# Performance work log

Measured on AMD Instinct MI355X. Metric: run time of the kernel, lower is better.

Reference implementation:

```python
import jax, jax.numpy as jnp
import numpy as np

N = 100000   # nodes
E = 1600000  # edges
IN, HID, OUT = 128, 128, 64


def setup_inputs() -> dict:
    key = jax.random.key(0)
    ks = jax.random.split(key, 8)
    x = jax.random.normal(ks[0], (N, IN), dtype=jnp.float32)
    edge_index = jax.random.randint(ks[1], (2, E), 0, N, dtype=jnp.int64)
    W1 = jax.random.normal(ks[2], (IN, HID), dtype=jnp.float32) * 0.05
    b1 = jnp.zeros((HID,), dtype=jnp.float32)
    W2 = jax.random.normal(ks[3], (HID, OUT), dtype=jnp.float32) * 0.05
    b2 = jnp.zeros((OUT,), dtype=jnp.float32)
    Wd = jax.random.normal(ks[4], (OUT, IN), dtype=jnp.float32) * 0.05
    bd = jnp.zeros((IN,), dtype=jnp.float32)
    return {"x": x, "edge_index": edge_index, "W1": W1, "b1": b1,
            "W2": W2, "b2": b2, "Wd": Wd, "bd": bd}


def _gcn_conv(x, src, dst, W, b):
    # PyG GCNConv: add self-loops, symmetric normalization D^-1/2 (A+I) D^-1/2,
    # messages flow src -> dst, aggregated by sum at dst.
    h = x @ W                                   # [N, F]
    ones = jnp.ones((src.shape[0],), x.dtype)
    deg = jax.ops.segment_sum(ones, dst, num_segments=N) + 1.0  # +1 for self-loop
    dinv = jax.lax.rsqrt(deg)                   # deg^-1/2, [N]
    coef = dinv[src] * dinv[dst]                # per-edge norm
    agg = jax.ops.segment_sum(h[src] * coef[:, None], dst, num_segments=N)
    agg = agg + h * (dinv * dinv)[:, None]      # self-loop contribution
    return agg + b


def reference(x, edge_index, W1, b1, W2, b2, Wd, bd):
    src, dst = edge_index[0], edge_index[1]
    h = jax.nn.relu(_gcn_conv(x, src, dst, W1, b1))
    # dropout in eval mode -> identity
    z = _gcn_conv(h, src, dst, W2, b2)          # [N, OUT] embedding
    x_recon = z @ Wd + bd                        # [N, IN]
    return (x_recon, z)
```

## Files before the change

kernel.cpp:

```cpp
#include <hip/hip_runtime.h>
#include <hip/hip_bf16.h>
#include <hip/hip_fp16.h>


#define TPB 256
#define CAP 64
#define BINCAP 220000
#define FILLW 112

typedef float v2f __attribute__((ext_vector_type(2)));


__device__ __forceinline__ unsigned short f2bf(float f) {
    unsigned u = __float_as_uint(f);
    unsigned r = u + 0x7fffu + ((u >> 16) & 1u);
    return (unsigned short)(r >> 16);
}
__device__ __forceinline__ float bf_lo(unsigned u) { return __uint_as_float(u << 16); }
__device__ __forceinline__ float bf_hi(unsigned u) { return __uint_as_float(u & 0xffff0000u); }


template <int K, int C, int TN, bool BIAS, bool INBF, bool OUTBF>
__device__ __forceinline__ void gemm_body(const void* __restrict__ Ap,
                                          const float* __restrict__ W,
                                          const float* __restrict__ bias,
                                          void* __restrict__ outp, int N, int bid,
                                          float* __restrict__ Ws) {
    constexpr int BM  = 128;
    constexpr int TM  = 8;
    constexpr int BK  = 32;
    constexpr int NCT = C / TN;
    static_assert(NCT * (BM / TM) == TPB, "thread layout");

    int tid = threadIdx.x;
    int tc = tid % NCT;
    int tr = tid / NCT;
    int c0 = tc * TN;
    int r0 = bid * BM + tr * TM;

    float acc[TM][TN] = {};

    for (int k0 = 0; k0 < K; k0 += BK) {
        __syncthreads();
        for (int i = tid * 4; i < BK * C; i += TPB * 4)
            *(float4*)&Ws[i] = *(const float4*)&W[k0 * C + i];
        __syncthreads();

        for (int k = 0; k < BK; k += 4) {
            float4 a[TM];
            uint2  au[TM];
#pragma unroll
            for (int i = 0; i < TM; ++i) {
                int r = r0 + i;
                if (r >= N) r = N - 1;
                if (INBF)
                    au[i] = *(const uint2*)((const unsigned short*)Ap + (size_t)r * K + k0 + k);
                else
                    a[i] = *(const float4*)((const float*)Ap + (size_t)r * K + k0 + k);
            }
#pragma unroll
            for (int kk = 0; kk < 4; ++kk) {
                float w[TN];
#pragma unroll
                for (int j = 0; j < TN; j += 4)
                    *(float4*)&w[j] = *(const float4*)&Ws[(k + kk) * C + c0 + j];
#pragma unroll
                for (int i = 0; i < TM; ++i) {
                    float av;
                    if (INBF) {
                        unsigned uu = (kk < 2) ? au[i].x : au[i].y;
                        av = (kk & 1) ? bf_hi(uu) : bf_lo(uu);
                    } else {
                        av = ((const float*)&a[i])[kk];
                    }
#pragma unroll
                    for (int j = 0; j < TN; ++j) acc[i][j] += av * w[j];
                }
            }
        }
    }

#pragma unroll
    for (int i = 0; i < TM; ++i) {
        int r = r0 + i;
        if (r >= N) continue;
        if (BIAS) {
#pragma unroll
            for (int j = 0; j < TN; ++j) acc[i][j] += bias[c0 + j];
        }
        if (OUTBF) {
            unsigned short* ob = (unsigned short*)outp + (size_t)r * C + c0;
            unsigned pk[TN / 2];
#pragma unroll
            for (int j = 0; j < TN; j += 2)
                pk[j / 2] = (unsigned)f2bf(acc[i][j]) | ((unsigned)f2bf(acc[i][j + 1]) << 16);
            if (TN == 8)      *(uint4*)ob = *(uint4*)pk;
            else if (TN == 4) *(uint2*)ob = *(uint2*)pk;
        } else {
            float* of = (float*)outp + (size_t)r * C + c0;
#pragma unroll
            for (int j = 0; j < TN; j += 4)
                *(float4*)&of[j] = *(float4*)&acc[i][j];
        }
    }
}

template <int K, int C, int TN, bool BIAS, bool INBF, bool OUTBF>
__global__ __launch_bounds__(TPB) void gemm_k(const void* __restrict__ Ap,
                                              const float* __restrict__ W,
                                              const float* __restrict__ bias,
                                              void* __restrict__ outp, int N) {
    __shared__ float Ws[32 * C];
    gemm_body<K, C, TN, BIAS, INBF, OUTBF>(Ap, W, bias, outp, N, blockIdx.x, Ws);
}


__global__ __launch_bounds__(TPB) void fused1_k(const float* __restrict__ x,
                                                const float* __restrict__ W1,
                                                unsigned* __restrict__ h1b,
                                                const int* __restrict__ src,
                                                const int* __restrict__ dst,
                                                uint2* __restrict__ binBuf,
                                                int* __restrict__ binCnt,
                                                int N, int E, int gb, unsigned M) {
    __shared__ float Ws[32 * 128];
    __shared__ int hist[8], gbase[8], lpos[8];
    if ((int)blockIdx.x < gb) {
        gemm_body<128, 128, 8, false, false, true>(x, W1, nullptr, h1b, N, blockIdx.x, Ws);
    } else {
        int bid = (int)blockIdx.x - gb;
        int tid = (int)threadIdx.x;
        if (tid < 8) { hist[tid] = 0; lpos[tid] = 0; }
        __syncthreads();

        int e0 = (bid * TPB + tid) * 8;
        int ne = E - e0; ne = ne > 8 ? 8 : (ne < 0 ? 0 : ne);
        int ss[8], dd[8], bb8[8];
        if (ne == 8) {
            int4 sa = *(const int4*)&src[e0];
            int4 sb = *(const int4*)&src[e0 + 4];
            int4 da = *(const int4*)&dst[e0];
            int4 db = *(const int4*)&dst[e0 + 4];
            ss[0]=sa.x; ss[1]=sa.y; ss[2]=sa.z; ss[3]=sa.w;
            ss[4]=sb.x; ss[5]=sb.y; ss[6]=sb.z; ss[7]=sb.w;
            dd[0]=da.x; dd[1]=da.y; dd[2]=da.z; dd[3]=da.w;
            dd[4]=db.x; dd[5]=db.y; dd[6]=db.z; dd[7]=db.w;
        } else {
            for (int q = 0; q < ne; ++q) { ss[q] = src[e0 + q]; dd[q] = dst[e0 + q]; }
        }
        for (int q = 0; q < ne; ++q) {
            bb8[q] = (int)(((unsigned long long)(unsigned)dd[q] * M) >> 32);
            atomicAdd(&hist[bb8[q]], 1);
        }
        __syncthreads();
        if (tid < 8) gbase[tid] = atomicAdd(&binCnt[tid], hist[tid]);
        __syncthreads();
        for (int q = 0; q < ne; ++q) {
            int b = bb8[q];
            int p = gbase[b] + atomicAdd(&lpos[b], 1);
            if (p < BINCAP)
                binBuf[(size_t)b * BINCAP + p] = make_uint2((unsigned)ss[q], (unsigned)dd[q]);
        }
    }
}


__global__ __launch_bounds__(TPB) void fill_k(const uint2* __restrict__ binBuf,
                                              const int* __restrict__ binCnt,
                                              int* __restrict__ cnt,
                                              unsigned* __restrict__ bucket, int N) {
    int bin = (int)blockIdx.x & 7;
    int w   = (int)blockIdx.x >> 3;
    int cb  = binCnt[bin];
    if (cb > BINCAP) cb = BINCAP;
    const uint2* eb = binBuf + (size_t)bin * BINCAP;

    for (int base = w * (TPB * 8); base < cb; base += FILLW * (TPB * 8)) {
        int e0 = base + (int)threadIdx.x * 8;
        if (e0 + 8 <= cb) {
            unsigned s[8], d[8];
#pragma unroll
            for (int q = 0; q < 8; q += 2) {
                uint4 t = *(const uint4*)&eb[e0 + q];
                s[q] = t.x; d[q] = t.y; s[q + 1] = t.z; d[q + 1] = t.w;
            }
            int rr[8];
#pragma unroll
            for (int q = 0; q < 8; ++q) rr[q] = atomicAdd(&cnt[(int)d[q]], 1);
#pragma unroll
            for (int q = 0; q < 8; ++q)
                if (rr[q] < CAP) bucket[(size_t)rr[q] * N + d[q]] = s[q];
        } else {
            int lim = e0 + 8 < cb ? e0 + 8 : cb;
            for (int e = e0; e < lim; ++e) {
                uint2 t = eb[e];
                int r = atomicAdd(&cnt[(int)t.y], 1);
                if (r < CAP) bucket[(size_t)r * N + t.y] = t.x;
            }
        }
    }
}


__global__ __launch_bounds__(TPB) void dinv_k(const int* __restrict__ cnt,
                                              float* __restrict__ dinv, int N) {
    int i = blockIdx.x * TPB + (int)threadIdx.x;
    if (i < N) dinv[i] = rsqrtf((float)cnt[i] + 1.0f);
}


template <int F2, bool RELU, bool OUTBF>
__global__ __launch_bounds__(TPB) void agg_k(const unsigned* __restrict__ h,
                                             const float* __restrict__ dinv,
                                             const int* __restrict__ cnt,
                                             const unsigned* __restrict__ bucket,
                                             const float* __restrict__ bias,
                                             void* __restrict__ outp, int N) {
    constexpr int NPB = TPB / F2;
    int ln = threadIdx.x / F2;
    int f2 = threadIdx.x % F2;
    int n  = blockIdx.x * NPB + ln;
    if (n >= N) return;

    int cfull = cnt[n];
    float di = dinv[n];
    const unsigned* hp = h + f2;
    unsigned us = hp[(size_t)n * F2];
    v2f acc;
    acc.x = bf_lo(us) * (di * di);
    acc.y = bf_hi(us) * (di * di);

    int cn = cfull < CAP ? cfull : CAP;
    const unsigned* bp = bucket + n;

    int nfull = cn & ~7;
    int s[8], sn2[8];
    if (nfull > 0) {
#pragma unroll
        for (int q = 0; q < 8; ++q) s[q] = (int)bp[(size_t)q * N];
    }
    for (int j = 0; j < nfull; ) {
        int jn = j + 8;
        bool more = jn < nfull;
        if (more) {
#pragma unroll
            for (int q = 0; q < 8; ++q) sn2[q] = (int)bp[(size_t)(jn + q) * N];
        }
        unsigned v[8];
        float ds[8];
#pragma unroll
        for (int q = 0; q < 8; ++q) {
            v[q]  = hp[(size_t)s[q] * F2];
            ds[q] = dinv[s[q]];
        }
#pragma unroll
        for (int q = 0; q < 8; ++q) {
            float c = ds[q] * di;
            v2f hv; hv.x = bf_lo(v[q]); hv.y = bf_hi(v[q]);
            acc += hv * c;
        }
        if (more) {
#pragma unroll
            for (int q = 0; q < 8; ++q) s[q] = sn2[q];
        }
        j = jn;
    }
    for (int j = nfull; j < cn; ++j) {
        int sx = (int)bp[(size_t)j * N];
        unsigned v = hp[(size_t)sx * F2];
        float c = dinv[sx] * di;
        acc.x += c * bf_lo(v);
        acc.y += c * bf_hi(v);
    }

    float rx = acc.x + bias[2 * f2];
    float ry = acc.y + bias[2 * f2 + 1];
    if (RELU) { rx = fmaxf(rx, 0.f); ry = fmaxf(ry, 0.f); }
    if (OUTBF) {
        unsigned pk = (unsigned)f2bf(rx) | ((unsigned)f2bf(ry) << 16);
        ((unsigned*)outp)[(size_t)n * F2 + f2] = pk;
    } else {
        v2f r; r.x = rx; r.y = ry;
        __builtin_nontemporal_store(r, (v2f*)outp + (size_t)n * F2 + f2);
    }
}


extern "C" void kernel_launch(void* const* d_in, const int* in_sizes, int n_in,
                              void* d_out, int out_size, void* d_ws, size_t ws_size,
                              hipStream_t stream) {
    const float* x    = (const float*)d_in[0];
    const int*   eidx = (const int*)d_in[1];
    const float* W1   = (const float*)d_in[2];
    const float* b1   = (const float*)d_in[3];
    const float* W2   = (const float*)d_in[4];
    const float* b2   = (const float*)d_in[5];
    const float* Wd   = (const float*)d_in[6];
    const float* bd   = (const float*)d_in[7];

    const int N = in_sizes[0] / 128;
    const int E = in_sizes[1] / 2;
    const int* src = eidx;
    const int* dst = eidx + E;

    size_t off = 0;
    auto alloc = [&](size_t bytes) {
        void* p = (char*)d_ws + off;
        off += (bytes + 255) & ~(size_t)255;
        return p;
    };
    int*      cnt     = (int*)alloc((size_t)N * 4);
    float*    dinv    = (float*)alloc((size_t)N * 4);
    unsigned* bucket  = (unsigned*)alloc((size_t)N * CAP * 4);
    unsigned* h1b     = (unsigned*)alloc((size_t)N * 64 * 4);
    unsigned* h2b     = (unsigned*)alloc((size_t)N * 32 * 4);
    unsigned* hrelu_b = (unsigned*)alloc((size_t)N * 64 * 4);
    int*      binCnt  = (int*)alloc(256);
    uint2*    binBuf  = (uint2*)hrelu_b;
    (void)ws_size;

    float* x_recon = (float*)d_out;
    float* z_out   = (float*)d_out + (size_t)N * 128;

    const int gb = (N + 127) / 128;
    const int bb = (E + TPB * 8 - 1) / (TPB * 8);
    const unsigned M = (unsigned)((8ULL << 32) / (unsigned)N);

    (void)hipMemsetAsync(cnt, 0, (size_t)N * 4, stream);
    (void)hipMemsetAsync(binCnt, 0, 256, stream);

    fused1_k<<<gb + bb, TPB, 0, stream>>>(x, W1, h1b, src, dst, binBuf, binCnt, N, E, gb, M);
    fill_k<<<8 * FILLW, TPB, 0, stream>>>(binBuf, binCnt, cnt, bucket, N);
    dinv_k<<<(N + TPB - 1) / TPB, TPB, 0, stream>>>(cnt, dinv, N);

    agg_k<64, true, true><<<(N + 3) / 4, TPB, 0, stream>>>(h1b, dinv, cnt, bucket, b1, hrelu_b, N);
    gemm_k<128, 64, 4, false, true, true><<<gb, TPB, 0, stream>>>(hrelu_b, W2, nullptr, h2b, N);
    agg_k<32, false, false><<<(N + 7) / 8, TPB, 0, stream>>>(h2b, dinv, cnt, bucket, b2, z_out, N);
    gemm_k<64, 128, 8, true, false, false><<<gb, TPB, 0, stream>>>(z_out, Wd, bd, x_recon, N);
}
```

Measured before the change: 470.2 us.

## Store neighbor buckets node-major and broadcast source indices via wave shuffles

The per-destination neighbor bucket moves from a slot-major [CAP][N] layout to a node-major [N][CAP] layout, in both the fill kernel and the aggregation kernel. In aggregation, each node's lanes now load the node's whole contiguous bucket row once and hand source indices to each other with __shfl. This replaces the repeated strided, broadcast loads of the old prefetch scheme, and the gather loop now works in chunks of 16 neighbours with guarded tails. In exchange, the fill-side scatter pattern changes, and the shuffle plus runtime indexing of the small row array adds some instruction overhead.

```diff
diff --git a/kernel.cpp b/kernel.cpp
--- a/kernel.cpp
+++ b/kernel.cpp
@@ -189,13 +189,13 @@
             for (int q = 0; q < 8; ++q) rr[q] = atomicAdd(&cnt[(int)d[q]], 1);
 #pragma unroll
             for (int q = 0; q < 8; ++q)
-                if (rr[q] < CAP) bucket[(size_t)rr[q] * N + d[q]] = s[q];
+                if (rr[q] < CAP) bucket[(size_t)d[q] * CAP + rr[q]] = s[q];
         } else {
             int lim = e0 + 8 < cb ? e0 + 8 : cb;
             for (int e = e0; e < lim; ++e) {
                 uint2 t = eb[e];
                 int r = atomicAdd(&cnt[(int)t.y], 1);
-                if (r < CAP) bucket[(size_t)r * N + t.y] = t.x;
+                if (r < CAP) bucket[(size_t)t.y * CAP + r] = t.x;
             }
         }
     }
@@ -217,10 +217,19 @@
                                              const float* __restrict__ bias,
                                              void* __restrict__ outp, int N) {
     constexpr int NPB = TPB / F2;
+    constexpr int NB  = CAP / F2;
     int ln = threadIdx.x / F2;
     int f2 = threadIdx.x % F2;
     int n  = blockIdx.x * NPB + ln;
     if (n >= N) return;
+
+    int lane = threadIdx.x & 63;
+    int lb   = lane - f2;
+
+    unsigned brow[NB];
+#pragma unroll
+    for (int k = 0; k < NB; ++k)
+        brow[k] = bucket[(size_t)n * CAP + k * F2 + f2];
 
     int cfull = cnt[n];
     float di = dinv[n];
@@ -231,46 +240,29 @@
     acc.y = bf_hi(us) * (di * di);
 
     int cn = cfull < CAP ? cfull : CAP;
-    const unsigned* bp = bucket + n;
-
-    int nfull = cn & ~7;
-    int s[8], sn2[8];
-    if (nfull > 0) {
-#pragma unroll
-        for (int q = 0; q < 8; ++q) s[q] = (int)bp[(size_t)q * N];
-    }
-    for (int j = 0; j < nfull; ) {
-        int jn = j + 8;
-        bool more = jn < nfull;
-        if (more) {
-#pragma unroll
-            for (int q = 0; q < 8; ++q) sn2[q] = (int)bp[(size_t)(jn + q) * N];
-        }
-        unsigned v[8];
-        float ds[8];
-#pragma unroll
-        for (int q = 0; q < 8; ++q) {
-            v[q]  = hp[(size_t)s[q] * F2];
-            ds[q] = dinv[s[q]];
-        }
-#pragma unroll
-        for (int q = 0; q < 8; ++q) {
-            float c = ds[q] * di;
-            v2f hv; hv.x = bf_lo(v[q]); hv.y = bf_hi(v[q]);
-            acc += hv * c;
-        }
-        if (more) {
-#pragma unroll
-            for (int q = 0; q < 8; ++q) s[q] = sn2[q];
-        }
-        j = jn;
-    }
-    for (int j = nfull; j < cn; ++j) {
-        int sx = (int)bp[(size_t)j * N];
-        unsigned v = hp[(size_t)sx * F2];
-        float c = dinv[sx] * di;
-        acc.x += c * bf_lo(v);
-        acc.y += c * bf_hi(v);
+
+    for (int j0 = 0; j0 < cn; j0 += 16) {
+        int m = cn - j0; m = m < 16 ? m : 16;
+        unsigned v[16];
+        float ds[16];
+#pragma unroll
+        for (int q = 0; q < 16; ++q) {
+            if (q < m) {
+                int jj = j0 + q;
+                unsigned bv = brow[jj / F2];
+                int s = __shfl((int)bv, lb + (jj & (F2 - 1)));
+                v[q]  = hp[(size_t)s * F2];
+                ds[q] = dinv[s];
+            }
+        }
+#pragma unroll
+        for (int q = 0; q < 16; ++q) {
+            if (q < m) {
+                float c = ds[q] * di;
+                v2f hv; hv.x = bf_lo(v[q]); hv.y = bf_hi(v[q]);
+                acc += hv * c;
+            }
+        }
     }
 
     float rx = acc.x + bias[2 * f2];
```

Result: slower. 490.4 us (+4.3%).

## Slice feature tables into column blocks and store buckets row-major per node

Applied to the files above, without the earlier changes.

The GEMMs now write their bf16 outputs as 8 column slices of [N, SU] each. The aggregation kernels map block index to (slice, node chunk), so each gather works over a smaller contiguous table that fits the cache better. The neighbour bucket layout moves from [CAP][N] to [N][CAP], so each node's source list is contiguous and read with nontemporal loads. In exchange, each slice block rereads cnt, dinv and the bucket row, which is 8x the index traffic, and each gather pulls 16 or 32 bytes per row instead of a full row.

```diff
diff --git a/kernel.cpp b/kernel.cpp
--- a/kernel.cpp
+++ b/kernel.cpp
@@ -20,7 +20,7 @@
 __device__ __forceinline__ float bf_hi(unsigned u) { return __uint_as_float(u & 0xffff0000u); }
 
 
-template <int K, int C, int TN, bool BIAS, bool INBF, bool OUTBF>
+template <int K, int C, int TN, bool BIAS, bool INBF, bool OUTBF, int SLICEU>
 __device__ __forceinline__ void gemm_body(const void* __restrict__ Ap,
                                           const float* __restrict__ W,
                                           const float* __restrict__ bias,
@@ -89,13 +89,23 @@
             for (int j = 0; j < TN; ++j) acc[i][j] += bias[c0 + j];
         }
         if (OUTBF) {
-            unsigned short* ob = (unsigned short*)outp + (size_t)r * C + c0;
             unsigned pk[TN / 2];
 #pragma unroll
             for (int j = 0; j < TN; j += 2)
                 pk[j / 2] = (unsigned)f2bf(acc[i][j]) | ((unsigned)f2bf(acc[i][j + 1]) << 16);
-            if (TN == 8)      *(uint4*)ob = *(uint4*)pk;
-            else if (TN == 4) *(uint2*)ob = *(uint2*)pk;
+            if (SLICEU > 0) {
+                constexpr int SUU = SLICEU > 0 ? SLICEU : 1;
+                int uidx0 = c0 / 2;
+                int slice = uidx0 / SUU;
+                int su0   = uidx0 % SUU;
+                unsigned* ob = (unsigned*)outp + (size_t)slice * N * SUU + (size_t)r * SUU + su0;
+                if (TN == 8)      *(uint4*)ob = *(uint4*)pk;
+                else if (TN == 4) *(uint2*)ob = *(uint2*)pk;
+            } else {
+                unsigned short* ob = (unsigned short*)outp + (size_t)r * C + c0;
+                if (TN == 8)      *(uint4*)ob = *(uint4*)pk;
+                else if (TN == 4) *(uint2*)ob = *(uint2*)pk;
+            }
         } else {
             float* of = (float*)outp + (size_t)r * C + c0;
 #pragma unroll
@@ -105,19 +115,19 @@
     }
 }
 
-template <int K, int C, int TN, bool BIAS, bool INBF, bool OUTBF>
+template <int K, int C, int TN, bool BIAS, bool INBF, bool OUTBF, int SLICEU>
 __global__ __launch_bounds__(TPB) void gemm_k(const void* __restrict__ Ap,
                                               const float* __restrict__ W,
                                               const float* __restrict__ bias,
                                               void* __restrict__ outp, int N) {
     __shared__ float Ws[32 * C];
-    gemm_body<K, C, TN, BIAS, INBF, OUTBF>(Ap, W, bias, outp, N, blockIdx.x, Ws);
+    gemm_body<K, C, TN, BIAS, INBF, OUTBF, SLICEU>(Ap, W, bias, outp, N, blockIdx.x, Ws);
 }
 
 
 __global__ __launch_bounds__(TPB) void fused1_k(const float* __restrict__ x,
                                                 const float* __restrict__ W1,
-                                                unsigned* __restrict__ h1b,
+                                                unsigned* __restrict__ h1t,
                                                 const int* __restrict__ src,
                                                 const int* __restrict__ dst,
                                                 uint2* __restrict__ binBuf,
@@ -126,7 +136,7 @@
     __shared__ float Ws[32 * 128];
     __shared__ int hist[8], gbase[8], lpos[8];
     if ((int)blockIdx.x < gb) {
-        gemm_body<128, 128, 8, false, false, true>(x, W1, nullptr, h1b, N, blockIdx.x, Ws);
+        gemm_body<128, 128, 8, false, false, true, 8>(x, W1, nullptr, h1t, N, blockIdx.x, Ws);
     } else {
         int bid = (int)blockIdx.x - gb;
         int tid = (int)threadIdx.x;
@@ -189,13 +199,13 @@
             for (int q = 0; q < 8; ++q) rr[q] = atomicAdd(&cnt[(int)d[q]], 1);
 #pragma unroll
             for (int q = 0; q < 8; ++q)
-                if (rr[q] < CAP) bucket[(size_t)rr[q] * N + d[q]] = s[q];
+                if (rr[q] < CAP) bucket[(size_t)d[q] * CAP + rr[q]] = s[q];
         } else {
             int lim = e0 + 8 < cb ? e0 + 8 : cb;
             for (int e = e0; e < lim; ++e) {
                 uint2 t = eb[e];
                 int r = atomicAdd(&cnt[(int)t.y], 1);
-                if (r < CAP) bucket[(size_t)r * N + t.y] = t.x;
+                if (r < CAP) bucket[(size_t)t.y * CAP + r] = t.x;
             }
         }
     }
@@ -209,55 +219,57 @@
 }
 
 
-template <int F2, bool RELU, bool OUTBF>
-__global__ __launch_bounds__(TPB) void agg_k(const unsigned* __restrict__ h,
-                                             const float* __restrict__ dinv,
-                                             const int* __restrict__ cnt,
-                                             const unsigned* __restrict__ bucket,
-                                             const float* __restrict__ bias,
-                                             void* __restrict__ outp, int N) {
-    constexpr int NPB = TPB / F2;
-    int ln = threadIdx.x / F2;
-    int f2 = threadIdx.x % F2;
-    int n  = blockIdx.x * NPB + ln;
+template <int SU, bool RELU, bool OUTBF>
+__global__ __launch_bounds__(TPB) void aggs_k(const unsigned* __restrict__ ht,
+                                              const float* __restrict__ dinv,
+                                              const int* __restrict__ cnt,
+                                              const unsigned* __restrict__ bucket,
+                                              const float* __restrict__ bias,
+                                              void* __restrict__ outp, int N) {
+    constexpr int NPB = TPB / SU;
+    int slice = (int)blockIdx.x & 7;
+    int chunk = (int)blockIdx.x >> 3;
+    int ln = (int)threadIdx.x / SU;
+    int fl = (int)threadIdx.x % SU;
+    int n  = chunk * NPB + ln;
     if (n >= N) return;
+
+    const unsigned* hs = ht + (size_t)slice * N * SU;
 
     int cfull = cnt[n];
     float di = dinv[n];
-    const unsigned* hp = h + f2;
-    unsigned us = hp[(size_t)n * F2];
-    v2f acc;
-    acc.x = bf_lo(us) * (di * di);
-    acc.y = bf_hi(us) * (di * di);
+    unsigned us = hs[(size_t)n * SU + fl];
+    float ax = bf_lo(us) * (di * di);
+    float ay = bf_hi(us) * (di * di);
 
     int cn = cfull < CAP ? cfull : CAP;
-    const unsigned* bp = bucket + n;
+    const unsigned* brow = bucket + (size_t)n * CAP;
 
     int nfull = cn & ~7;
     int s[8], sn2[8];
     if (nfull > 0) {
 #pragma unroll
-        for (int q = 0; q < 8; ++q) s[q] = (int)bp[(size_t)q * N];
+        for (int q = 0; q < 8; ++q) s[q] = (int)__builtin_nontemporal_load(&brow[q]);
     }
     for (int j = 0; j < nfull; ) {
         int jn = j + 8;
         bool more = jn < nfull;
         if (more) {
 #pragma unroll
-            for (int q = 0; q < 8; ++q) sn2[q] = (int)bp[(size_t)(jn + q) * N];
+            for (int q = 0; q < 8; ++q) sn2[q] = (int)__builtin_nontemporal_load(&brow[jn + q]);
         }
         unsigned v[8];
         float ds[8];
 #pragma unroll
         for (int q = 0; q < 8; ++q) {
-            v[q]  = hp[(size_t)s[q] * F2];
+            v[q]  = hs[(size_t)s[q] * SU + fl];
             ds[q] = dinv[s[q]];
         }
 #pragma unroll
         for (int q = 0; q < 8; ++q) {
             float c = ds[q] * di;
-            v2f hv; hv.x = bf_lo(v[q]); hv.y = bf_hi(v[q]);
-            acc += hv * c;
+            ax += c * bf_lo(v[q]);
+            ay += c * bf_hi(v[q]);
         }
         if (more) {
 #pragma unroll
@@ -266,22 +278,23 @@
         j = jn;
     }
     for (int j = nfull; j < cn; ++j) {
-        int sx = (int)bp[(size_t)j * N];
-        unsigned v = hp[(size_t)sx * F2];
+        int sx = (int)brow[j];
+        unsigned v = hs[(size_t)sx * SU + fl];
         float c = dinv[sx] * di;
-        acc.x += c * bf_lo(v);
-        acc.y += c * bf_hi(v);
-    }
-
-    float rx = acc.x + bias[2 * f2];
-    float ry = acc.y + bias[2 * f2 + 1];
+        ax += c * bf_lo(v);
+        ay += c * bf_hi(v);
+    }
+
+    int uidx = slice * SU + fl;
+    float rx = ax + bias[2 * uidx];
+    float ry = ay + bias[2 * uidx + 1];
     if (RELU) { rx = fmaxf(rx, 0.f); ry = fmaxf(ry, 0.f); }
     if (OUTBF) {
         unsigned pk = (unsigned)f2bf(rx) | ((unsigned)f2bf(ry) << 16);
-        ((unsigned*)outp)[(size_t)n * F2 + f2] = pk;
+        ((unsigned*)outp)[(size_t)n * (8 * SU) + uidx] = pk;
     } else {
         v2f r; r.x = rx; r.y = ry;
-        __builtin_nontemporal_store(r, (v2f*)outp + (size_t)n * F2 + f2);
+        __builtin_nontemporal_store(r, (v2f*)outp + (size_t)n * (8 * SU) + uidx);
     }
 }
 
@@ -312,8 +325,8 @@
     int*      cnt     = (int*)alloc((size_t)N * 4);
     float*    dinv    = (float*)alloc((size_t)N * 4);
     unsigned* bucket  = (unsigned*)alloc((size_t)N * CAP * 4);
-    unsigned* h1b     = (unsigned*)alloc((size_t)N * 64 * 4);
-    unsigned* h2b     = (unsigned*)alloc((size_t)N * 32 * 4);
+    unsigned* h1t     = (unsigned*)alloc((size_t)N * 64 * 4);
+    unsigned* h2t     = (unsigned*)alloc((size_t)N * 32 * 4);
     unsigned* hrelu_b = (unsigned*)alloc((size_t)N * 64 * 4);
     int*      binCnt  = (int*)alloc(256);
     uint2*    binBuf  = (uint2*)hrelu_b;
@@ -329,12 +342,14 @@
     (void)hipMemsetAsync(cnt, 0, (size_t)N * 4, stream);
     (void)hipMemsetAsync(binCnt, 0, 256, stream);
 
-    fused1_k<<<gb + bb, TPB, 0, stream>>>(x, W1, h1b, src, dst, binBuf, binCnt, N, E, gb, M);
+    fused1_k<<<gb + bb, TPB, 0, stream>>>(x, W1, h1t, src, dst, binBuf, binCnt, N, E, gb, M);
     fill_k<<<8 * FILLW, TPB, 0, stream>>>(binBuf, binCnt, cnt, bucket, N);
     dinv_k<<<(N + TPB - 1) / TPB, TPB, 0, stream>>>(cnt, dinv, N);
 
-    agg_k<64, true, true><<<(N + 3) / 4, TPB, 0, stream>>>(h1b, dinv, cnt, bucket, b1, hrelu_b, N);
-    gemm_k<128, 64, 4, false, true, true><<<gb, TPB, 0, stream>>>(hrelu_b, W2, nullptr, h2b, N);
-    agg_k<32, false, false><<<(N + 7) / 8, TPB, 0, stream>>>(h2b, dinv, cnt, bucket, b2, z_out, N);
-    gemm_k<64, 128, 8, true, false, false><<<gb, TPB, 0, stream>>>(z_out, Wd, bd, x_recon, N);
-}
+    aggs_k<8, true, true><<<8 * ((N + 31) / 32), TPB, 0, stream>>>(
+        h1t, dinv, cnt, bucket, b1, hrelu_b, N);
+    gemm_k<128, 64, 4, false, true, true, 4><<<gb, TPB, 0, stream>>>(hrelu_b, W2, nullptr, h2t, N);
+    aggs_k<4, false, false><<<8 * ((N + 63) / 64), TPB, 0, stream>>>(
+        h2t, dinv, cnt, bucket, b2, z_out, N);
+    gemm_k<64, 128, 8, true, false, false, 0><<<gb, TPB, 0, stream>>>(z_out, Wd, bd, x_recon, N);
+}
```

Result: slower. 728.6 us (+55.0%).

## Fuse edge binning into GEMM launch and fold decoder GEMM into second aggregation

Applied to the files above, without the earlier changes.

The two-pass edge binning (histogram into a staging buffer, then a separate fill kernel) is replaced by a single pass inside the first GEMM launch. Each fill block scans a span of edges and keeps only those whose destination falls in its bin, so src/dst are read eight times in exchange for no staging buffer and one fewer launch. The second aggregation kernel now also computes the decoder GEMM from the z values it holds in shared memory, which removes a kernel launch and the global re-read of z. The fused decoder reads Wd from global per thread without staging it in shared memory, and the edge scan assumes E is a multiple of 4 for its int4 loads.

```diff
diff --git a/kernel.cpp b/kernel.cpp
--- a/kernel.cpp
+++ b/kernel.cpp
@@ -5,7 +5,6 @@
 
 #define TPB 256
 #define CAP 64
-#define BINCAP 220000
 #define FILLW 112
 
 typedef float v2f __attribute__((ext_vector_type(2)));
@@ -120,82 +119,31 @@
                                                 unsigned* __restrict__ h1b,
                                                 const int* __restrict__ src,
                                                 const int* __restrict__ dst,
-                                                uint2* __restrict__ binBuf,
-                                                int* __restrict__ binCnt,
-                                                int N, int E, int gb, unsigned M) {
+                                                int* __restrict__ cnt,
+                                                unsigned* __restrict__ bucket,
+                                                int N, int E, int span, unsigned M) {
     __shared__ float Ws[32 * 128];
-    __shared__ int hist[8], gbase[8], lpos[8];
-    if ((int)blockIdx.x < gb) {
-        gemm_body<128, 128, 8, false, false, true>(x, W1, nullptr, h1b, N, blockIdx.x, Ws);
+    constexpr int FB = 8 * FILLW;
+    int bid = (int)blockIdx.x;
+    if (bid >= FB) {
+        gemm_body<128, 128, 8, false, false, true>(x, W1, nullptr, h1b, N, bid - FB, Ws);
     } else {
-        int bid = (int)blockIdx.x - gb;
-        int tid = (int)threadIdx.x;
-        if (tid < 8) { hist[tid] = 0; lpos[tid] = 0; }
-        __syncthreads();
-
-        int e0 = (bid * TPB + tid) * 8;
-        int ne = E - e0; ne = ne > 8 ? 8 : (ne < 0 ? 0 : ne);
-        int ss[8], dd[8], bb8[8];
-        if (ne == 8) {
-            int4 sa = *(const int4*)&src[e0];
-            int4 sb = *(const int4*)&src[e0 + 4];
-            int4 da = *(const int4*)&dst[e0];
-            int4 db = *(const int4*)&dst[e0 + 4];
-            ss[0]=sa.x; ss[1]=sa.y; ss[2]=sa.z; ss[3]=sa.w;
-            ss[4]=sb.x; ss[5]=sb.y; ss[6]=sb.z; ss[7]=sb.w;
-            dd[0]=da.x; dd[1]=da.y; dd[2]=da.z; dd[3]=da.w;
-            dd[4]=db.x; dd[5]=db.y; dd[6]=db.z; dd[7]=db.w;
-        } else {
-            for (int q = 0; q < ne; ++q) { ss[q] = src[e0 + q]; dd[q] = dst[e0 + q]; }
-        }
-        for (int q = 0; q < ne; ++q) {
-            bb8[q] = (int)(((unsigned long long)(unsigned)dd[q] * M) >> 32);
-            atomicAdd(&hist[bb8[q]], 1);
-        }
-        __syncthreads();
-        if (tid < 8) gbase[tid] = atomicAdd(&binCnt[tid], hist[tid]);
-        __syncthreads();
-        for (int q = 0; q < ne; ++q) {
-            int b = bb8[q];
-            int p = gbase[b] + atomicAdd(&lpos[b], 1);
-            if (p < BINCAP)
-                binBuf[(size_t)b * BINCAP + p] = make_uint2((unsigned)ss[q], (unsigned)dd[q]);
-        }
-    }
-}
-
-
-__global__ __launch_bounds__(TPB) void fill_k(const uint2* __restrict__ binBuf,
-                                              const int* __restrict__ binCnt,
-                                              int* __restrict__ cnt,
-                                              unsigned* __restrict__ bucket, int N) {
-    int bin = (int)blockIdx.x & 7;
-    int w   = (int)blockIdx.x >> 3;
-    int cb  = binCnt[bin];
-    if (cb > BINCAP) cb = BINCAP;
-    const uint2* eb = binBuf + (size_t)bin * BINCAP;
-
-    for (int base = w * (TPB * 8); base < cb; base += FILLW * (TPB * 8)) {
-        int e0 = base + (int)threadIdx.x * 8;
-        if (e0 + 8 <= cb) {
-            unsigned s[8], d[8];
-#pragma unroll
-            for (int q = 0; q < 8; q += 2) {
-                uint4 t = *(const uint4*)&eb[e0 + q];
-                s[q] = t.x; d[q] = t.y; s[q + 1] = t.z; d[q + 1] = t.w;
-            }
-            int rr[8];
-#pragma unroll
-            for (int q = 0; q < 8; ++q) rr[q] = atomicAdd(&cnt[(int)d[q]], 1);
-#pragma unroll
-            for (int q = 0; q < 8; ++q)
-                if (rr[q] < CAP) bucket[(size_t)rr[q] * N + d[q]] = s[q];
-        } else {
-            int lim = e0 + 8 < cb ? e0 + 8 : cb;
-            for (int e = e0; e < lim; ++e) {
-                uint2 t = eb[e];
-                int r = atomicAdd(&cnt[(int)t.y], 1);
-                if (r < CAP) bucket[(size_t)r * N + t.y] = t.x;
+        int bin = bid & 7;
+        int w   = bid >> 3;
+        int lo  = w * span;
+        int hi  = lo + span; if (hi > E) hi = E;
+        for (int e0 = lo + (int)threadIdx.x * 4; e0 < hi; e0 += TPB * 4) {
+            int4 d4 = *(const int4*)&dst[e0];
+            int4 s4 = *(const int4*)&src[e0];
+            int dd[4] = {d4.x, d4.y, d4.z, d4.w};
+            int ss[4] = {s4.x, s4.y, s4.z, s4.w};
+#pragma unroll
+            for (int q = 0; q < 4; ++q) {
+                int b = (int)(((unsigned long long)(unsigned)dd[q] * M) >> 32);
+                if (b == bin) {
+                    int r = atomicAdd(&cnt[dd[q]], 1);
+                    if (r < CAP) bucket[(size_t)r * N + dd[q]] = (unsigned)ss[q];
+                }
             }
         }
     }
@@ -286,6 +234,98 @@
 }
 
 
+__global__ __launch_bounds__(TPB) void agg2g_k(const unsigned* __restrict__ h,
+                                               const float* __restrict__ dinv,
+                                               const int* __restrict__ cnt,
+                                               const unsigned* __restrict__ bucket,
+                                               const float* __restrict__ bias,
+                                               const float* __restrict__ Wd,
+                                               const float* __restrict__ bd,
+                                               float* __restrict__ z_out,
+                                               float* __restrict__ x_recon, int N) {
+    constexpr int F2 = 32, NPB = TPB / F2;
+    __shared__ float zl[NPB][64];
+    int ln = (int)threadIdx.x / F2;
+    int f2 = (int)threadIdx.x % F2;
+    int n  = blockIdx.x * NPB + ln;
+
+    if (n < N) {
+        int cfull = cnt[n];
+        float di = dinv[n];
+        const unsigned* hp = h + f2;
+        unsigned us = hp[(size_t)n * F2];
+        v2f acc;
+        acc.x = bf_lo(us) * (di * di);
+        acc.y = bf_hi(us) * (di * di);
+
+        int cn = cfull < CAP ? cfull : CAP;
+        const unsigned* bp = bucket + n;
+
+        int nfull = cn & ~7;
+        int s[8], sn2[8];
+        if (nfull > 0) {
+#pragma unroll
+            for (int q = 0; q < 8; ++q) s[q] = (int)bp[(size_t)q * N];
+        }
+        for (int j = 0; j < nfull; ) {
+            int jn = j + 8;
+            bool more = jn < nfull;
+            if (more) {
+#pragma unroll
+                for (int q = 0; q < 8; ++q) sn2[q] = (int)bp[(size_t)(jn + q) * N];
+            }
+            unsigned v[8];
+            float ds[8];
+#pragma unroll
+            for (int q = 0; q < 8; ++q) {
+                v[q]  = hp[(size_t)s[q] * F2];
+                ds[q] = dinv[s[q]];
+            }
+#pragma unroll
+            for (int q = 0; q < 8; ++q) {
+                float c = ds[q] * di;
+                v2f hv; hv.x = bf_lo(v[q]); hv.y = bf_hi(v[q]);
+                acc += hv * c;
+            }
+            if (more) {
+#pragma unroll
+                for (int q = 0; q < 8; ++q) s[q] = sn2[q];
+            }
+            j = jn;
+        }
+        for (int j = nfull; j < cn; ++j) {
+            int sx = (int)bp[(size_t)j * N];
+            unsigned v = hp[(size_t)sx * F2];
+            float c = dinv[sx] * di;
+            acc.x += c * bf_lo(v);
+            acc.y += c * bf_hi(v);
+        }
+
+        float rx = acc.x + bias[2 * f2];
+        float ry = acc.y + bias[2 * f2 + 1];
+        v2f r; r.x = rx; r.y = ry;
+        __builtin_nontemporal_store(r, (v2f*)z_out + (size_t)n * F2 + f2);
+        *(v2f*)&zl[ln][2 * f2] = r;
+    }
+    __syncthreads();
+
+    int dn = (int)threadIdx.x / 32;
+    int c0 = ((int)threadIdx.x % 32) * 4;
+    int nn = blockIdx.x * NPB + dn;
+    if (nn < N) {
+        float a0 = bd[c0], a1 = bd[c0 + 1], a2 = bd[c0 + 2], a3 = bd[c0 + 3];
+#pragma unroll 4
+        for (int k = 0; k < 64; ++k) {
+            float zv = zl[dn][k];
+            float4 w = *(const float4*)&Wd[k * 128 + c0];
+            a0 += zv * w.x; a1 += zv * w.y; a2 += zv * w.z; a3 += zv * w.w;
+        }
+        float4 o; o.x = a0; o.y = a1; o.z = a2; o.w = a3;
+        *(float4*)&x_recon[(size_t)nn * 128 + c0] = o;
+    }
+}
+
+
 extern "C" void kernel_launch(void* const* d_in, const int* in_sizes, int n_in,
                               void* d_out, int out_size, void* d_ws, size_t ws_size,
                               hipStream_t stream) {
@@ -315,26 +355,24 @@
     unsigned* h1b     = (unsigned*)alloc((size_t)N * 64 * 4);
     unsigned* h2b     = (unsigned*)alloc((size_t)N * 32 * 4);
     unsigned* hrelu_b = (unsigned*)alloc((size_t)N * 64 * 4);
-    int*      binCnt  = (int*)alloc(256);
-    uint2*    binBuf  = (uint2*)hrelu_b;
     (void)ws_size;
 
     float* x_recon = (float*)d_out;
     float* z_out   = (float*)d_out + (size_t)N * 128;
 
     const int gb = (N + 127) / 128;
-    const int bb = (E + TPB * 8 - 1) / (TPB * 8);
+    int span = (E + FILLW - 1) / FILLW;
+    span = (span + TPB * 4 - 1) & ~(TPB * 4 - 1);
     const unsigned M = (unsigned)((8ULL << 32) / (unsigned)N);
 
     (void)hipMemsetAsync(cnt, 0, (size_t)N * 4, stream);
-    (void)hipMemsetAsync(binCnt, 0, 256, stream);
-
-    fused1_k<<<gb + bb, TPB, 0, stream>>>(x, W1, h1b, src, dst, binBuf, binCnt, N, E, gb, M);
-    fill_k<<<8 * FILLW, TPB, 0, stream>>>(binBuf, binCnt, cnt, bucket, N);
+
+    fused1_k<<<8 * FILLW + gb, TPB, 0, stream>>>(x, W1, h1b, src, dst, cnt, bucket,
+                                                 N, E, span, M);
     dinv_k<<<(N + TPB - 1) / TPB, TPB, 0, stream>>>(cnt, dinv, N);
 
     agg_k<64, true, true><<<(N + 3) / 4, TPB, 0, stream>>>(h1b, dinv, cnt, bucket, b1, hrelu_b, N);
     gemm_k<128, 64, 4, false, true, true><<<gb, TPB, 0, stream>>>(hrelu_b, W2, nullptr, h2b, N);
-    agg_k<32, false, false><<<(N + 7) / 8, TPB, 0, stream>>>(h2b, dinv, cnt, bucket, b2, z_out, N);
-    gemm_k<64, 128, 8, true, false, false><<<gb, TPB, 0, stream>>>(z_out, Wd, bd, x_recon, N);
-}
+    agg2g_k<<<(N + 7) / 8, TPB, 0, stream>>>(h2b, dinv, cnt, bucket, b2, Wd, bd,
+                                             z_out, x_recon, N);
+}
```

Result: slower. 497.3 us (+5.8%).
